# Kernel tuning notes

Hardware: AMD Instinct MI355X
Metric: run time of the kernel (lower is better)

## Reference

```python
import jax, jax.numpy as jnp
import numpy as np

N_NODES = 50000
N_EDGES = 1600000
IN_DIM, HID, OUT = 128, 64, 32


def _glorot(key, fan_in, fan_out):
    s = 1.0 / np.sqrt(fan_in)
    return jax.random.uniform(key, (fan_in, fan_out), jnp.float32, -s, s)


def setup_inputs() -> dict:
    key = jax.random.key(0)
    ks = jax.random.split(key, 12)
    x = jax.random.normal(ks[0], (N_NODES, IN_DIM), jnp.float32)
    edge_index = jax.random.randint(ks[1], (2, N_EDGES), 0, N_NODES, jnp.int32)
    inp = {"x": x, "edge_index": edge_index}
    # 4 SAGEConv layers: (in->hid), (hid->hid), (hid->hid), (hid->hid)
    dims = [(IN_DIM, HID), (HID, HID), (HID, HID), (HID, HID)]
    names = ["1a", "1b", "2a", "2b"]
    for i, ((di, do), nm) in enumerate(zip(dims, names)):
        k1, k2 = jax.random.split(ks[2 + i])
        inp[f"W{nm}_l"] = _glorot(k1, di, do)       # neighbor transform (with bias)
        inp[f"b{nm}"] = jnp.zeros((do,), jnp.float32)
        inp[f"W{nm}_r"] = _glorot(k2, di, do)       # root/self transform (no bias)
    inp["Wlin"] = _glorot(ks[10], HID, OUT)
    inp["blin"] = jnp.zeros((OUT,), jnp.float32)
    return inp


def _sage(h, src, dst, Wl, bl, Wr, n_nodes):
    # SAGEConv: out = mean_{j in N(i)} x_j @ Wl + bl + x_i @ Wr
    msg = h[src]                                                    # [E, D] gather
    ssum = jax.ops.segment_sum(msg, dst, num_segments=n_nodes)     # [N, D] scatter-add
    cnt = jax.ops.segment_sum(jnp.ones((src.shape[0], 1), h.dtype), dst, num_segments=n_nodes)
    agg = ssum / jnp.maximum(cnt, 1.0)                              # mean; 0 for isolated nodes
    return agg @ Wl + bl + h @ Wr


def reference(x, edge_index, W1a_l, b1a, W1a_r, W1b_l, b1b, W1b_r,
              W2a_l, b2a, W2a_r, W2b_l, b2b, W2b_r, Wlin, blin):
    src, dst = edge_index[0], edge_index[1]
    n = x.shape[0]
    # conv1 = GraphSAGE(2 layers): sage -> relu -> sage ; then outer F.relu
    h = jax.nn.relu(_sage(x, src, dst, W1a_l, b1a, W1a_r, n))
    h = jax.nn.relu(_sage(h, src, dst, W1b_l, b1b, W1b_r, n))
    # conv2 = GraphSAGE(2 layers): sage -> relu -> sage (no final act)
    h = jax.nn.relu(_sage(h, src, dst, W2a_l, b2a, W2a_r, n))
    h = _sage(h, src, dst, W2b_l, b2b, W2b_r, n)
    return h @ Wlin + blin
```

## Files before the change

### kernel.cpp

```cpp
#include <hip/hip_runtime.h>
#include <hip/hip_fp16.h>


#define CHUNK 4096
#define EPT 16
#define SLICE_W 512
#define MAXS 128

__global__ __launch_bounds__(256) void bucket_scatter_direct(
    const int* __restrict__ e32, int* __restrict__ scnt,
    unsigned* __restrict__ bedge, int E, int S, int bcap)
{
    __shared__ int h[MAXS];
    __shared__ int hb[MAXS];
    const int tid = threadIdx.x, b = blockIdx.x;
    for (int i = tid; i < S; i += 256) h[i] = 0;
    __syncthreads();
    const int lo = b * CHUNK;
    unsigned v[EPT];
    int sl[EPT], rk[EPT];
    #pragma unroll
    for (int k = 0; k < EPT; ++k) {
        const int e = lo + k * 256 + tid;
        sl[k] = -1;
        if (e < E) {
            const int s = e32[e], d = e32[E + e];
            v[k]  = ((unsigned)s << 16) | (unsigned)d;
            sl[k] = d >> 9;
            rk[k] = atomicAdd(&h[sl[k]], 1);
        }
    }
    __syncthreads();
    for (int i = tid; i < S; i += 256)
        hb[i] = h[i] ? atomicAdd(&scnt[i], h[i]) : 0;
    __syncthreads();
    #pragma unroll
    for (int k = 0; k < EPT; ++k) {
        if (sl[k] >= 0) {
            const int pos = hb[sl[k]] + rk[k];
            if (pos < bcap)
                bedge[(size_t)sl[k] * bcap + pos] = v[k];
        }
    }
}

__global__ __launch_bounds__(1024) void csr_fill2(
    const unsigned* __restrict__ bedge, const int* __restrict__ scnt,
    int* __restrict__ rbeg, int* __restrict__ deg,
    float* __restrict__ inv, unsigned short* __restrict__ adj,
    int N, int bcap)
{
    __shared__ int cnt[SLICE_W];
    __shared__ int sc[SLICE_W];
    const int s = blockIdx.x, tid = threadIdx.x;
    const int n = min(scnt[s], bcap);
    const size_t base = (size_t)s * bcap;
    if (tid < SLICE_W) cnt[tid] = 0;
    __syncthreads();
    for (int i = tid; i < n; i += 1024)
        atomicAdd(&cnt[bedge[base + i] & (SLICE_W - 1)], 1);
    __syncthreads();
    if (tid < SLICE_W) sc[tid] = cnt[tid];
    __syncthreads();
    for (int off = 1; off < SLICE_W; off <<= 1) {
        int a = 0;
        if (tid < SLICE_W && tid >= off) a = sc[tid - off];
        __syncthreads();
        if (tid < SLICE_W) sc[tid] += a;
        __syncthreads();
    }
    if (tid < SLICE_W) {
        const int c = cnt[tid];
        const int excl = sc[tid] - c;
        const int node = (s << 9) + tid;
        if (node < N) {
            rbeg[node] = (int)base + excl;
            deg[node]  = c;
            inv[node]  = 1.0f / (float)(c > 0 ? c : 1);
        }
        cnt[tid] = excl;
    }
    __syncthreads();
    for (int i = tid; i < n; i += 1024) {
        const unsigned v = bedge[base + i];
        const int p = atomicAdd(&cnt[v & (SLICE_W - 1)], 1);
        adj[base + p] = (unsigned short)(v >> 16);
    }
}

__global__ __launch_bounds__(256) void compose(
    const float* __restrict__ Wl, const float* __restrict__ Wr,
    const float* __restrict__ b2, const float* __restrict__ Wlin,
    const float* __restrict__ blin, float* __restrict__ C1,
    float* __restrict__ C2, float* __restrict__ cb)
{
    __shared__ float Ws[64 * 32];
    const int tid = threadIdx.x;
    for (int i = tid * 4; i < 64 * 32; i += 1024)
        *(float4*)&Ws[i] = *(const float4*)&Wlin[i];
    __syncthreads();
    for (int idx = tid; idx < 64 * 32; idx += 256) {
        const int r = idx >> 5, c = idx & 31;
        float s1 = 0.f, s2 = 0.f;
        #pragma unroll 8
        for (int k = 0; k < 64; ++k) {
            const float w = Ws[k * 32 + c];
            s1 += Wl[r * 64 + k] * w;
            s2 += Wr[r * 64 + k] * w;
        }
        C1[idx] = s1;
        C2[idx] = s2;
    }
    if (tid < 32) {
        float s = blin[tid];
        #pragma unroll 8
        for (int k = 0; k < 64; ++k) s += b2[k] * Ws[k * 32 + tid];
        cb[tid] = s;
    }
}

template<bool RELU>
__global__ __launch_bounds__(256) void gather_fused(
    const __half* __restrict__ t, const unsigned short* __restrict__ adj,
    const int* __restrict__ rbeg, const int* __restrict__ deg,
    const float* __restrict__ inv, const __half* __restrict__ u,
    float* __restrict__ out, int N)
{
    const int node = (blockIdx.x * 256 + threadIdx.x) >> 6;
    const int lane = threadIdx.x & 63;
    const int grp  = lane >> 3;
    const int d0   = (lane & 7) * 8;
    if (node >= N) return;
    const int beg = rbeg[node];
    const int end = beg + deg[node];
    float a[8] = {0.f, 0.f, 0.f, 0.f, 0.f, 0.f, 0.f, 0.f};
    int j = beg + grp;
    for (; j + 8 < end; j += 16) {
        const int n0 = adj[j], n1 = adj[j + 8];
        const float4 p0 = *(const float4*)(t + (size_t)n0 * 64 + d0);
        const float4 p1 = *(const float4*)(t + (size_t)n1 * 64 + d0);
        const __half2* h0 = (const __half2*)&p0;
        const __half2* h1 = (const __half2*)&p1;
        #pragma unroll
        for (int k = 0; k < 4; ++k) {
            float2 f0 = __half22float2(h0[k]);
            float2 f1 = __half22float2(h1[k]);
            a[2 * k]     += f0.x + f1.x;
            a[2 * k + 1] += f0.y + f1.y;
        }
    }
    if (j < end) {
        const float4 p0 = *(const float4*)(t + (size_t)adj[j] * 64 + d0);
        const __half2* h0 = (const __half2*)&p0;
        #pragma unroll
        for (int k = 0; k < 4; ++k) {
            float2 f0 = __half22float2(h0[k]);
            a[2 * k]     += f0.x;
            a[2 * k + 1] += f0.y;
        }
    }
    #pragma unroll
    for (int k = 0; k < 8; ++k) {
        a[k] += __shfl_xor(a[k], 8);
        a[k] += __shfl_xor(a[k], 16);
        a[k] += __shfl_xor(a[k], 32);
    }
    if (grp == 0) {
        const float vi = inv[node];
        const float4 uv = *(const float4*)(u + (size_t)node * 64 + d0);
        const __half2* uh = (const __half2*)&uv;
        float4 o0, o1;
        {
            float2 g0 = __half22float2(uh[0]);
            float2 g1 = __half22float2(uh[1]);
            float2 g2 = __half22float2(uh[2]);
            float2 g3 = __half22float2(uh[3]);
            o0.x = g0.x + a[0] * vi; o0.y = g0.y + a[1] * vi;
            o0.z = g1.x + a[2] * vi; o0.w = g1.y + a[3] * vi;
            o1.x = g2.x + a[4] * vi; o1.y = g2.y + a[5] * vi;
            o1.z = g3.x + a[6] * vi; o1.w = g3.y + a[7] * vi;
        }
        if (RELU) {
            o0.x = fmaxf(o0.x, 0.f); o0.y = fmaxf(o0.y, 0.f);
            o0.z = fmaxf(o0.z, 0.f); o0.w = fmaxf(o0.w, 0.f);
            o1.x = fmaxf(o1.x, 0.f); o1.y = fmaxf(o1.y, 0.f);
            o1.z = fmaxf(o1.z, 0.f); o1.w = fmaxf(o1.w, 0.f);
        }
        *(float4*)(out + (size_t)node * 64 + d0)     = o0;
        *(float4*)(out + (size_t)node * 64 + d0 + 4) = o1;
    }
}

__global__ __launch_bounds__(256) void gather32(
    const __half* __restrict__ t, const unsigned short* __restrict__ adj,
    const int* __restrict__ rbeg, const int* __restrict__ deg,
    const float* __restrict__ inv, const __half* __restrict__ u,
    float* __restrict__ out, int N)
{
    const int node = (blockIdx.x * 256 + threadIdx.x) >> 6;
    const int lane = threadIdx.x & 63;
    const int grp  = lane >> 2;
    const int d0   = (lane & 3) * 8;
    if (node >= N) return;
    const int beg = rbeg[node];
    const int end = beg + deg[node];
    float a[8] = {0.f, 0.f, 0.f, 0.f, 0.f, 0.f, 0.f, 0.f};
    int j = beg + grp;
    for (; j + 16 < end; j += 32) {
        const int n0 = adj[j], n1 = adj[j + 16];
        const float4 p0 = *(const float4*)(t + (size_t)n0 * 32 + d0);
        const float4 p1 = *(const float4*)(t + (size_t)n1 * 32 + d0);
        const __half2* h0 = (const __half2*)&p0;
        const __half2* h1 = (const __half2*)&p1;
        #pragma unroll
        for (int k = 0; k < 4; ++k) {
            float2 f0 = __half22float2(h0[k]);
            float2 f1 = __half22float2(h1[k]);
            a[2 * k]     += f0.x + f1.x;
            a[2 * k + 1] += f0.y + f1.y;
        }
    }
    if (j < end) {
        const float4 p0 = *(const float4*)(t + (size_t)adj[j] * 32 + d0);
        const __half2* h0 = (const __half2*)&p0;
        #pragma unroll
        for (int k = 0; k < 4; ++k) {
            float2 f0 = __half22float2(h0[k]);
            a[2 * k]     += f0.x;
            a[2 * k + 1] += f0.y;
        }
    }
    #pragma unroll
    for (int k = 0; k < 8; ++k) {
        a[k] += __shfl_xor(a[k], 4);
        a[k] += __shfl_xor(a[k], 8);
        a[k] += __shfl_xor(a[k], 16);
        a[k] += __shfl_xor(a[k], 32);
    }
    if (grp == 0) {
        const float vi = inv[node];
        const float4 uv = *(const float4*)(u + (size_t)node * 32 + d0);
        const __half2* uh = (const __half2*)&uv;
        float4 o0, o1;
        float2 g0 = __half22float2(uh[0]);
        float2 g1 = __half22float2(uh[1]);
        float2 g2 = __half22float2(uh[2]);
        float2 g3 = __half22float2(uh[3]);
        o0.x = g0.x + a[0] * vi; o0.y = g0.y + a[1] * vi;
        o0.z = g1.x + a[2] * vi; o0.w = g1.y + a[3] * vi;
        o1.x = g2.x + a[4] * vi; o1.y = g2.y + a[5] * vi;
        o1.z = g3.x + a[6] * vi; o1.w = g3.y + a[7] * vi;
        *(float4*)(out + (size_t)node * 32 + d0)     = o0;
        *(float4*)(out + (size_t)node * 32 + d0 + 4) = o1;
    }
}

template<int K, int DOUT>
__global__ __launch_bounds__(256) void mm_dual(
    const float* __restrict__ A, const float* __restrict__ Wl,
    const float* __restrict__ Wr, const float* __restrict__ bias,
    __half* __restrict__ T, __half* __restrict__ U, int M)
{
    constexpr int CT = DOUT / 16;
    __shared__ float As[64][36];
    __shared__ float Wls[32 * DOUT];
    __shared__ float Wrs[32 * DOUT];
    const int tid  = threadIdx.x;
    const int row0 = blockIdx.x * 64;
    const int tx = tid & 15, ty = tid >> 4;
    float accT[4][CT], accU[4][CT];
    #pragma unroll
    for (int r = 0; r < 4; ++r)
        #pragma unroll
        for (int c = 0; c < CT; ++c) { accT[r][c] = 0.f; accU[r][c] = 0.f; }

    for (int kc = 0; kc < K; kc += 32) {
        if (kc) __syncthreads();
        for (int i = tid * 4; i < 64 * 32; i += 1024) {
            int r = i >> 5, c = i & 31;
            int gr = row0 + r;
            float4 v = make_float4(0.f, 0.f, 0.f, 0.f);
            if (gr < M) v = *(const float4*)&A[(size_t)gr * K + kc + c];
            *(float4*)&As[r][c] = v;
        }
        for (int i = tid * 4; i < 32 * DOUT; i += 1024) {
            *(float4*)&Wls[i] = *(const float4*)&Wl[kc * DOUT + i];
            *(float4*)&Wrs[i] = *(const float4*)&Wr[kc * DOUT + i];
        }
        __syncthreads();
        #pragma unroll 4
        for (int kk = 0; kk < 32; ++kk) {
            float a[4];
            #pragma unroll
            for (int r = 0; r < 4; ++r) a[r] = As[ty * 4 + r][kk];
            float bl[CT], br[CT];
            #pragma unroll
            for (int c = 0; c < CT; ++c) {
                bl[c] = Wls[kk * DOUT + tx * CT + c];
                br[c] = Wrs[kk * DOUT + tx * CT + c];
            }
            #pragma unroll
            for (int r = 0; r < 4; ++r)
                #pragma unroll
                for (int c = 0; c < CT; ++c) {
                    accT[r][c] += a[r] * bl[c];
                    accU[r][c] += a[r] * br[c];
                }
        }
    }

    float bv[CT];
    #pragma unroll
    for (int c = 0; c < CT; ++c) bv[c] = bias[tx * CT + c];
    #pragma unroll
    for (int r = 0; r < 4; ++r) {
        int gr = row0 + ty * 4 + r;
        if (gr >= M) continue;
        if (CT == 4) {
            union { int2 v; __half2 h[2]; } tp;
            tp.h[0] = __floats2half2_rn(accT[r][0], accT[r][1]);
            tp.h[1] = __floats2half2_rn(accT[r][2], accT[r][3]);
            *(int2*)&T[(size_t)gr * DOUT + tx * 4] = tp.v;
            union { int2 v; __half2 h[2]; } up;
            up.h[0] = __floats2half2_rn(accU[r][0] + bv[0], accU[r][1] + bv[1]);
            up.h[1] = __floats2half2_rn(accU[r][2] + bv[2], accU[r][3] + bv[3]);
            *(int2*)&U[(size_t)gr * DOUT + tx * 4] = up.v;
        } else {
            union { int v; __half2 h; } tp;
            tp.h = __floats2half2_rn(accT[r][0], accT[r][1]);
            *(int*)&T[(size_t)gr * DOUT + tx * 2] = tp.v;
            union { int v; __half2 h; } up;
            up.h = __floats2half2_rn(accU[r][0] + bv[0], accU[r][1] + bv[1]);
            *(int*)&U[(size_t)gr * DOUT + tx * 2] = up.v;
        }
    }
}

extern "C" void kernel_launch(void* const* d_in, const int* in_sizes, int n_in,
                              void* d_out, int out_size, void* d_ws, size_t ws_size,
                              hipStream_t stream) {
    const float* x     = (const float*)d_in[0];
    const int*   ei    = (const int*)  d_in[1];
    const float* W1a_l = (const float*)d_in[2];
    const float* b1a   = (const float*)d_in[3];
    const float* W1a_r = (const float*)d_in[4];
    const float* W1b_l = (const float*)d_in[5];
    const float* b1b   = (const float*)d_in[6];
    const float* W1b_r = (const float*)d_in[7];
    const float* W2a_l = (const float*)d_in[8];
    const float* b2a   = (const float*)d_in[9];
    const float* W2a_r = (const float*)d_in[10];
    const float* W2b_l = (const float*)d_in[11];
    const float* b2b   = (const float*)d_in[12];
    const float* W2b_r = (const float*)d_in[13];
    const float* Wlin  = (const float*)d_in[14];
    const float* blin  = (const float*)d_in[15];

    const int N = in_sizes[0] / 128;
    const int E = in_sizes[1] / 2;
    const int S = (N + SLICE_W - 1) / SLICE_W;
    const int B = (E + CHUNK - 1) / CHUNK;
    const int bcap = (((E + S - 1) / S) + 2048 + 15) & ~15;

    size_t o = 0;
    auto take = [&](size_t bytes) -> void* {
        void* p = (char*)d_ws + o;
        o += (bytes + 255) & ~(size_t)255;
        return p;
    };
    int*            scnt  = (int*)     take((size_t)S * 4);
    unsigned*       bedge = (unsigned*)take((size_t)S * bcap * 4);
    int*            rbeg  = (int*)     take((size_t)N * 4);
    int*            deg   = (int*)     take((size_t)N * 4);
    float*          inv   = (float*)   take((size_t)N * 4);
    unsigned short* adj   = (unsigned short*)take((size_t)S * bcap * 2);
    __half*         t     = (__half*)  take((size_t)N * 64 * 2);
    __half*         u     = (__half*)  take((size_t)N * 64 * 2);
    float*          hA    = (float*)   take((size_t)N * 64 * 4);
    float*          hB    = (float*)   take((size_t)N * 64 * 4);
    float*          C1    = (float*)   take((size_t)64 * 32 * 4);
    float*          C2    = (float*)   take((size_t)64 * 32 * 4);
    float*          cb    = (float*)   take((size_t)32 * 4);
    (void)ws_size; (void)n_in; (void)out_size;

    const int mb = (N + 63) / 64;
    const int gb = (N * 64 + 255) / 256;

    hipMemsetAsync(scnt, 0, (size_t)S * 4, stream);
    bucket_scatter_direct<<<B, 256, 0, stream>>>(ei, scnt, bedge, E, S, bcap);
    csr_fill2<<<S, 1024, 0, stream>>>(bedge, scnt, rbeg, deg, inv, adj, N, bcap);
    compose<<<1, 256, 0, stream>>>(W2b_l, W2b_r, b2b, Wlin, blin, C1, C2, cb);

    mm_dual<128, 64><<<mb, 256, 0, stream>>>(x, W1a_l, W1a_r, b1a, t, u, N);
    gather_fused<true><<<gb, 256, 0, stream>>>(t, adj, rbeg, deg, inv, u, hA, N);
    mm_dual<64, 64><<<mb, 256, 0, stream>>>(hA, W1b_l, W1b_r, b1b, t, u, N);
    gather_fused<true><<<gb, 256, 0, stream>>>(t, adj, rbeg, deg, inv, u, hB, N);
    mm_dual<64, 64><<<mb, 256, 0, stream>>>(hB, W2a_l, W2a_r, b2a, t, u, N);
    gather_fused<true><<<gb, 256, 0, stream>>>(t, adj, rbeg, deg, inv, u, hA, N);
    mm_dual<64, 32><<<mb, 256, 0, stream>>>(hA, C1, C2, cb, t, u, N);
    gather32<<<gb, 256, 0, stream>>>(t, adj, rbeg, deg, inv, u, (float*)d_out, N);
}
```

Measured before the change: 256.6 us.

## Split 64-wide gather tables into two 32-wide halves for cache residency

The matmul now writes the neighbor-transformed features as two separate 32-column half-precision tables. Each 64-wide aggregation becomes two 32-wide gather passes, so the randomly accessed table (N×32 fp16, about 3.2MB) is more likely to stay resident in cache. Adjacency and root-term loads use nontemporal hints so they do not evict it. The cost is reading the adjacency list twice per layer and launching extra kernels.

Measured after the change: 331.5 us. 1.29x slower.

```diff
diff --git a/kernel.cpp b/kernel.cpp
--- a/kernel.cpp
+++ b/kernel.cpp
@@ -6,6 +6,8 @@
 #define EPT 16
 #define SLICE_W 512
 #define MAXS 128
+
+typedef float v4f __attribute__((ext_vector_type(4)));
 
 __global__ __launch_bounds__(256) void bucket_scatter_direct(
     const int* __restrict__ e32, int* __restrict__ scnt,
@@ -119,79 +121,8 @@
     }
 }
 
-template<bool RELU>
-__global__ __launch_bounds__(256) void gather_fused(
-    const __half* __restrict__ t, const unsigned short* __restrict__ adj,
-    const int* __restrict__ rbeg, const int* __restrict__ deg,
-    const float* __restrict__ inv, const __half* __restrict__ u,
-    float* __restrict__ out, int N)
-{
-    const int node = (blockIdx.x * 256 + threadIdx.x) >> 6;
-    const int lane = threadIdx.x & 63;
-    const int grp  = lane >> 3;
-    const int d0   = (lane & 7) * 8;
-    if (node >= N) return;
-    const int beg = rbeg[node];
-    const int end = beg + deg[node];
-    float a[8] = {0.f, 0.f, 0.f, 0.f, 0.f, 0.f, 0.f, 0.f};
-    int j = beg + grp;
-    for (; j + 8 < end; j += 16) {
-        const int n0 = adj[j], n1 = adj[j + 8];
-        const float4 p0 = *(const float4*)(t + (size_t)n0 * 64 + d0);
-        const float4 p1 = *(const float4*)(t + (size_t)n1 * 64 + d0);
-        const __half2* h0 = (const __half2*)&p0;
-        const __half2* h1 = (const __half2*)&p1;
-        #pragma unroll
-        for (int k = 0; k < 4; ++k) {
-            float2 f0 = __half22float2(h0[k]);
-            float2 f1 = __half22float2(h1[k]);
-            a[2 * k]     += f0.x + f1.x;
-            a[2 * k + 1] += f0.y + f1.y;
-        }
-    }
-    if (j < end) {
-        const float4 p0 = *(const float4*)(t + (size_t)adj[j] * 64 + d0);
-        const __half2* h0 = (const __half2*)&p0;
-        #pragma unroll
-        for (int k = 0; k < 4; ++k) {
-            float2 f0 = __half22float2(h0[k]);
-            a[2 * k]     += f0.x;
-            a[2 * k + 1] += f0.y;
-        }
-    }
-    #pragma unroll
-    for (int k = 0; k < 8; ++k) {
-        a[k] += __shfl_xor(a[k], 8);
-        a[k] += __shfl_xor(a[k], 16);
-        a[k] += __shfl_xor(a[k], 32);
-    }
-    if (grp == 0) {
-        const float vi = inv[node];
-        const float4 uv = *(const float4*)(u + (size_t)node * 64 + d0);
-        const __half2* uh = (const __half2*)&uv;
-        float4 o0, o1;
-        {
-            float2 g0 = __half22float2(uh[0]);
-            float2 g1 = __half22float2(uh[1]);
-            float2 g2 = __half22float2(uh[2]);
-            float2 g3 = __half22float2(uh[3]);
-            o0.x = g0.x + a[0] * vi; o0.y = g0.y + a[1] * vi;
-            o0.z = g1.x + a[2] * vi; o0.w = g1.y + a[3] * vi;
-            o1.x = g2.x + a[4] * vi; o1.y = g2.y + a[5] * vi;
-            o1.z = g3.x + a[6] * vi; o1.w = g3.y + a[7] * vi;
-        }
-        if (RELU) {
-            o0.x = fmaxf(o0.x, 0.f); o0.y = fmaxf(o0.y, 0.f);
-            o0.z = fmaxf(o0.z, 0.f); o0.w = fmaxf(o0.w, 0.f);
-            o1.x = fmaxf(o1.x, 0.f); o1.y = fmaxf(o1.y, 0.f);
-            o1.z = fmaxf(o1.z, 0.f); o1.w = fmaxf(o1.w, 0.f);
-        }
-        *(float4*)(out + (size_t)node * 64 + d0)     = o0;
-        *(float4*)(out + (size_t)node * 64 + d0 + 4) = o1;
-    }
-}
-
-__global__ __launch_bounds__(256) void gather32(
+template<bool RELU, int STRIDE>
+__global__ __launch_bounds__(256) void gather_half(
     const __half* __restrict__ t, const unsigned short* __restrict__ adj,
     const int* __restrict__ rbeg, const int* __restrict__ deg,
     const float* __restrict__ inv, const __half* __restrict__ u,
@@ -207,7 +138,8 @@
     float a[8] = {0.f, 0.f, 0.f, 0.f, 0.f, 0.f, 0.f, 0.f};
     int j = beg + grp;
     for (; j + 16 < end; j += 32) {
-        const int n0 = adj[j], n1 = adj[j + 16];
+        const int n0 = __builtin_nontemporal_load(adj + j);
+        const int n1 = __builtin_nontemporal_load(adj + j + 16);
         const float4 p0 = *(const float4*)(t + (size_t)n0 * 32 + d0);
         const float4 p1 = *(const float4*)(t + (size_t)n1 * 32 + d0);
         const __half2* h0 = (const __half2*)&p0;
@@ -221,7 +153,8 @@
         }
     }
     if (j < end) {
-        const float4 p0 = *(const float4*)(t + (size_t)adj[j] * 32 + d0);
+        const int nl = __builtin_nontemporal_load(adj + j);
+        const float4 p0 = *(const float4*)(t + (size_t)nl * 32 + d0);
         const __half2* h0 = (const __half2*)&p0;
         #pragma unroll
         for (int k = 0; k < 4; ++k) {
@@ -239,19 +172,26 @@
     }
     if (grp == 0) {
         const float vi = inv[node];
-        const float4 uv = *(const float4*)(u + (size_t)node * 32 + d0);
-        const __half2* uh = (const __half2*)&uv;
+        union { v4f v; __half2 h[4]; } uu;
+        uu.v = __builtin_nontemporal_load(
+            (const v4f*)(u + (size_t)node * STRIDE + d0));
         float4 o0, o1;
-        float2 g0 = __half22float2(uh[0]);
-        float2 g1 = __half22float2(uh[1]);
-        float2 g2 = __half22float2(uh[2]);
-        float2 g3 = __half22float2(uh[3]);
+        float2 g0 = __half22float2(uu.h[0]);
+        float2 g1 = __half22float2(uu.h[1]);
+        float2 g2 = __half22float2(uu.h[2]);
+        float2 g3 = __half22float2(uu.h[3]);
         o0.x = g0.x + a[0] * vi; o0.y = g0.y + a[1] * vi;
         o0.z = g1.x + a[2] * vi; o0.w = g1.y + a[3] * vi;
         o1.x = g2.x + a[4] * vi; o1.y = g2.y + a[5] * vi;
         o1.z = g3.x + a[6] * vi; o1.w = g3.y + a[7] * vi;
-        *(float4*)(out + (size_t)node * 32 + d0)     = o0;
-        *(float4*)(out + (size_t)node * 32 + d0 + 4) = o1;
+        if (RELU) {
+            o0.x = fmaxf(o0.x, 0.f); o0.y = fmaxf(o0.y, 0.f);
+            o0.z = fmaxf(o0.z, 0.f); o0.w = fmaxf(o0.w, 0.f);
+            o1.x = fmaxf(o1.x, 0.f); o1.y = fmaxf(o1.y, 0.f);
+            o1.z = fmaxf(o1.z, 0.f); o1.w = fmaxf(o1.w, 0.f);
+        }
+        *(float4*)(out + (size_t)node * STRIDE + d0)     = o0;
+        *(float4*)(out + (size_t)node * STRIDE + d0 + 4) = o1;
     }
 }
 
@@ -259,7 +199,8 @@
 __global__ __launch_bounds__(256) void mm_dual(
     const float* __restrict__ A, const float* __restrict__ Wl,
     const float* __restrict__ Wr, const float* __restrict__ bias,
-    __half* __restrict__ T, __half* __restrict__ U, int M)
+    __half* __restrict__ TL, __half* __restrict__ TH,
+    __half* __restrict__ U, int M)
 {
     constexpr int CT = DOUT / 16;
     __shared__ float As[64][36];
@@ -317,10 +258,12 @@
         int gr = row0 + ty * 4 + r;
         if (gr >= M) continue;
         if (CT == 4) {
+            __half* Td = (tx < 8) ? TL : TH;
+            const int tcol = (tx * 4) & 31;
             union { int2 v; __half2 h[2]; } tp;
             tp.h[0] = __floats2half2_rn(accT[r][0], accT[r][1]);
             tp.h[1] = __floats2half2_rn(accT[r][2], accT[r][3]);
-            *(int2*)&T[(size_t)gr * DOUT + tx * 4] = tp.v;
+            *(int2*)&Td[(size_t)gr * 32 + tcol] = tp.v;
             union { int2 v; __half2 h[2]; } up;
             up.h[0] = __floats2half2_rn(accU[r][0] + bv[0], accU[r][1] + bv[1]);
             up.h[1] = __floats2half2_rn(accU[r][2] + bv[2], accU[r][3] + bv[3]);
@@ -328,7 +271,7 @@
         } else {
             union { int v; __half2 h; } tp;
             tp.h = __floats2half2_rn(accT[r][0], accT[r][1]);
-            *(int*)&T[(size_t)gr * DOUT + tx * 2] = tp.v;
+            *(int*)&TL[(size_t)gr * 32 + tx * 2] = tp.v;
             union { int v; __half2 h; } up;
             up.h = __floats2half2_rn(accU[r][0] + bv[0], accU[r][1] + bv[1]);
             *(int*)&U[(size_t)gr * DOUT + tx * 2] = up.v;
@@ -374,7 +317,8 @@
     int*            deg   = (int*)     take((size_t)N * 4);
     float*          inv   = (float*)   take((size_t)N * 4);
     unsigned short* adj   = (unsigned short*)take((size_t)S * bcap * 2);
-    __half*         t     = (__half*)  take((size_t)N * 64 * 2);
+    __half*         tL    = (__half*)  take((size_t)N * 32 * 2);
+    __half*         tH    = (__half*)  take((size_t)N * 32 * 2);
     __half*         u     = (__half*)  take((size_t)N * 64 * 2);
     float*          hA    = (float*)   take((size_t)N * 64 * 4);
     float*          hB    = (float*)   take((size_t)N * 64 * 4);
@@ -391,12 +335,15 @@
     csr_fill2<<<S, 1024, 0, stream>>>(bedge, scnt, rbeg, deg, inv, adj, N, bcap);
     compose<<<1, 256, 0, stream>>>(W2b_l, W2b_r, b2b, Wlin, blin, C1, C2, cb);
 
-    mm_dual<128, 64><<<mb, 256, 0, stream>>>(x, W1a_l, W1a_r, b1a, t, u, N);
-    gather_fused<true><<<gb, 256, 0, stream>>>(t, adj, rbeg, deg, inv, u, hA, N);
-    mm_dual<64, 64><<<mb, 256, 0, stream>>>(hA, W1b_l, W1b_r, b1b, t, u, N);
-    gather_fused<true><<<gb, 256, 0, stream>>>(t, adj, rbeg, deg, inv, u, hB, N);
-    mm_dual<64, 64><<<mb, 256, 0, stream>>>(hB, W2a_l, W2a_r, b2a, t, u, N);
-    gather_fused<true><<<gb, 256, 0, stream>>>(t, adj, rbeg, deg, inv, u, hA, N);
-    mm_dual<64, 32><<<mb, 256, 0, stream>>>(hA, C1, C2, cb, t, u, N);
-    gather32<<<gb, 256, 0, stream>>>(t, adj, rbeg, deg, inv, u, (float*)d_out, N);
-}
+    mm_dual<128, 64><<<mb, 256, 0, stream>>>(x, W1a_l, W1a_r, b1a, tL, tH, u, N);
+    gather_half<true, 64><<<gb, 256, 0, stream>>>(tL, adj, rbeg, deg, inv, u,      hA,      N);
+    gather_half<true, 64><<<gb, 256, 0, stream>>>(tH, adj, rbeg, deg, inv, u + 32, hA + 32, N);
+    mm_dual<64, 64><<<mb, 256, 0, stream>>>(hA, W1b_l, W1b_r, b1b, tL, tH, u, N);
+    gather_half<true, 64><<<gb, 256, 0, stream>>>(tL, adj, rbeg, deg, inv, u,      hB,      N);
+    gather_half<true, 64><<<gb, 256, 0, stream>>>(tH, adj, rbeg, deg, inv, u + 32, hB + 32, N);
+    mm_dual<64, 64><<<mb, 256, 0, stream>>>(hB, W2a_l, W2a_r, b2a, tL, tH, u, N);
+    gather_half<true, 64><<<gb, 256, 0, stream>>>(tL, adj, rbeg, deg, inv, u,      hA,      N);
+    gather_half<true, 64><<<gb, 256, 0, stream>>>(tH, adj, rbeg, deg, inv, u + 32, hA + 32, N);
+    mm_dual<64, 32><<<mb, 256, 0, stream>>>(hA, C1, C2, cb, tL, tH, u, N);
+    gather_half<false, 32><<<gb, 256, 0, stream>>>(tL, adj, rbeg, deg, inv, u, (float*)d_out, N);
+}
```
